# Kernel tuning notes

Measured on AMD Instinct MI355X. Metric: run time of the kernel, lower is better.

Reference implementation:

```python
import jax, jax.numpy as jnp
import numpy as np

NUM_HEADS = 16
HEAD_DIM = 64  # att_output_dim // num_heads = 1024 // 16


def setup_inputs() -> dict:
    key = jax.random.key(0)
    ks = jax.random.split(key, 7)
    B, S, D_IN, D_OUT = 4, 2048, 1024, 1024
    std = 1.0 / np.sqrt(D_IN)
    return {
        "ts10_input": jax.random.normal(ks[0], (B, S, D_IN), dtype=jnp.float32),
        "Wq": jax.random.uniform(ks[1], (D_IN, D_OUT), jnp.float32, -std, std),
        "bq": jax.random.uniform(ks[2], (D_OUT,), jnp.float32, -std, std),
        "Wk": jax.random.uniform(ks[3], (D_IN, D_OUT), jnp.float32, -std, std),
        "bk": jax.random.uniform(ks[4], (D_OUT,), jnp.float32, -std, std),
        "Wv": jax.random.uniform(ks[5], (D_IN, D_OUT), jnp.float32, -std, std),
        "bv": jax.random.uniform(ks[6], (D_OUT,), jnp.float32, -std, std),
        "mask": 1,
    }


def reference(ts10_input, Wq, bq, Wk, bk, Wv, bv, mask):
    B, S, _ = ts10_input.shape
    H, Dh = NUM_HEADS, HEAD_DIM

    def split_heads(x):  # (B,S,H*Dh) -> (B,H,S,Dh)
        return x.reshape(B, S, H, Dh).transpose(0, 2, 1, 3)

    q = split_heads(ts10_input @ Wq + bq)
    k = split_heads(ts10_input @ Wk + bk)
    v = split_heads(ts10_input @ Wv + bv)

    scores = jnp.einsum("bhqd,bhkd->bhqk", q, k) / jnp.sqrt(jnp.float32(Dh))
    if mask:
        causal = jnp.tril(jnp.ones((S, S), dtype=bool))  # keep lower triangle incl diag
        scores = jnp.where(causal, scores, -jnp.inf)
    probs = jax.nn.softmax(scores, axis=-1)
    ctx = jnp.einsum("bhqk,bhkd->bhqd", probs, v)
    return ctx.transpose(0, 2, 1, 3).reshape(B, S, H * Dh)
```

## Files before the change

### kernel.cpp

```cpp
#include <hip/hip_runtime.h>

typedef __bf16 bf16x8 __attribute__((ext_vector_type(8)));
typedef __bf16 bf16x4 __attribute__((ext_vector_type(4)));
typedef short s16x4 __attribute__((ext_vector_type(4)));
typedef float f32x4 __attribute__((ext_vector_type(4)));
typedef unsigned short u16x8 __attribute__((ext_vector_type(8)));
typedef unsigned short u16x4 __attribute__((ext_vector_type(4)));
typedef unsigned int u32x2 __attribute__((ext_vector_type(2)));
typedef unsigned int __attribute__((address_space(1))) as1_uint;
typedef unsigned int __attribute__((address_space(3))) as3_uint;

#define S_LEN 2048
#define NB 4
#define NH 16
#define HD 64
#define DM 1024

#define Q_SCALE 0.18033688011112042f

__device__ __forceinline__ unsigned short f2bf(float f) {
  union { float f; unsigned int u; } v; v.f = f;
  unsigned int r = v.u + 0x7fffu + ((v.u >> 16) & 1u);
  return (unsigned short)(r >> 16);
}

__device__ __forceinline__ unsigned int fbits(float f) {
  union { float f; unsigned int u; } v; v.f = f;
  return v.u;
}

__device__ __forceinline__ f32x4 mfma16(u16x4 a, u16x4 b, f32x4 c) {
#if __has_builtin(__builtin_amdgcn_mfma_f32_16x16x16_bf16)
  return __builtin_amdgcn_mfma_f32_16x16x16_bf16(
      __builtin_bit_cast(bf16x4, a), __builtin_bit_cast(bf16x4, b), c, 0, 0, 0);
#else
  return __builtin_amdgcn_mfma_f32_16x16x16bf16_1k(
      __builtin_bit_cast(s16x4, a), __builtin_bit_cast(s16x4, b), c, 0, 0, 0);
#endif
}

__global__ __launch_bounds__(256) void cvt_x(const float* __restrict__ x,
                                             unsigned short* __restrict__ xb) {
  int i = (blockIdx.x * 256 + threadIdx.x) * 8;
  f32x4 a = *(const f32x4*)(x + i);
  f32x4 b = *(const f32x4*)(x + i + 4);
  u16x8 o;
  o[0] = f2bf(a[0]); o[1] = f2bf(a[1]); o[2] = f2bf(a[2]); o[3] = f2bf(a[3]);
  o[4] = f2bf(b[0]); o[5] = f2bf(b[1]); o[6] = f2bf(b[2]); o[7] = f2bf(b[3]);
  *(u16x8*)(xb + i) = o;
}

__global__ __launch_bounds__(256) void cvt_wt(const float* __restrict__ Wq,
                                              const float* __restrict__ Wk,
                                              const float* __restrict__ Wv,
                                              unsigned short* __restrict__ wt) {
  const float* W = (blockIdx.z == 0) ? Wq : (blockIdx.z == 1) ? Wk : Wv;
  unsigned short* WT = wt + (size_t)blockIdx.z * DM * DM;
  __shared__ float tile[32][33];
  int tx = threadIdx.x & 31, ty = threadIdx.x >> 5;
  int k0 = blockIdx.x * 32, n0 = blockIdx.y * 32;
#pragma unroll
  for (int i = 0; i < 4; ++i)
    tile[ty + 8 * i][tx] = W[(size_t)(k0 + ty + 8 * i) * DM + n0 + tx];
  __syncthreads();
#pragma unroll
  for (int i = 0; i < 4; ++i)
    WT[(size_t)(n0 + ty + 8 * i) * DM + k0 + tx] = f2bf(tile[tx][ty + 8 * i]);
}

__global__ __launch_bounds__(256) void qkv_gemm(const unsigned short* __restrict__ xb,
                                                const unsigned short* __restrict__ wt,
                                                const float* __restrict__ bq,
                                                const float* __restrict__ bk,
                                                const float* __restrict__ bv,
                                                unsigned short* __restrict__ qo,
                                                unsigned short* __restrict__ ko,
                                                unsigned short* __restrict__ vto) {
  const int z = blockIdx.z;
  const unsigned short* WT = wt + (size_t)z * DM * DM;
  const float* bias = (z == 0) ? bq : (z == 1) ? bk : bv;
  const int m0 = blockIdx.x * 128;
  const int n0 = blockIdx.y * 128;
  __shared__ __align__(16) unsigned short Al[128 * 32];
  __shared__ __align__(16) unsigned short Bl[128 * 32];
  const int tid = threadIdx.x;
  const int wave = tid >> 6, lane = tid & 63, quad = lane >> 4, lw = lane & 15;
  const int wm = (wave >> 1) * 64, wn = (wave & 1) * 64;

  f32x4 acc[4][4];
#pragma unroll
  for (int mt = 0; mt < 4; ++mt)
#pragma unroll
    for (int nt = 0; nt < 4; ++nt) acc[mt][nt] = (f32x4){0.f, 0.f, 0.f, 0.f};

  for (int k0 = 0; k0 < DM; k0 += 32) {
    __syncthreads();
#pragma unroll
    for (int i = 0; i < 2; ++i) {
      int c = i * 256 + tid;
      int row = c >> 2;
      int scn = (c & 3) ^ ((row >> 1) & 3);
      const unsigned short* ga = xb + (size_t)(m0 + row) * DM + k0 + scn * 8;
      __builtin_amdgcn_global_load_lds((const as1_uint*)ga, (as3_uint*)(Al + c * 8), 16, 0, 0);
      const unsigned short* gb = WT + (size_t)(n0 + row) * DM + k0 + scn * 8;
      __builtin_amdgcn_global_load_lds((const as1_uint*)gb, (as3_uint*)(Bl + c * 8), 16, 0, 0);
    }
    __syncthreads();
    bf16x8 af[4], bfr[4];
#pragma unroll
    for (int mt = 0; mt < 4; ++mt) {
      int r = wm + mt * 16 + lw;
      af[mt] = *(const bf16x8*)(Al + r * 32 + (quad ^ ((r >> 1) & 3)) * 8);
    }
#pragma unroll
    for (int nt = 0; nt < 4; ++nt) {
      int r = wn + nt * 16 + lw;
      bfr[nt] = *(const bf16x8*)(Bl + r * 32 + (quad ^ ((r >> 1) & 3)) * 8);
    }
#pragma unroll
    for (int mt = 0; mt < 4; ++mt)
#pragma unroll
      for (int nt = 0; nt < 4; ++nt)
        acc[mt][nt] = __builtin_amdgcn_mfma_f32_16x16x32_bf16(af[mt], bfr[nt], acc[mt][nt], 0, 0, 0);
  }

  float bias4[4];
#pragma unroll
  for (int nt = 0; nt < 4; ++nt) bias4[nt] = bias[n0 + wn + nt * 16 + lw];

  if (z < 2) {
    unsigned short* dst = (z == 0) ? qo : ko;
    const float sc = (z == 0) ? Q_SCALE : 1.0f;
#pragma unroll
    for (int mt = 0; mt < 4; ++mt) {
#pragma unroll
      for (int nt = 0; nt < 4; ++nt) {
        int n = n0 + wn + nt * 16 + lw;
        int h = n >> 6, d = n & 63;
#pragma unroll
        for (int r = 0; r < 4; ++r) {
          int m = m0 + wm + mt * 16 + quad * 4 + r;
          int b = m >> 11, s = m & 2047;
          dst[((size_t)(b * NH + h) * S_LEN + s) * HD + d] = f2bf((acc[mt][nt][r] + bias4[nt]) * sc);
        }
      }
    }
  } else {
#pragma unroll
    for (int mt = 0; mt < 4; ++mt) {
#pragma unroll
      for (int nt = 0; nt < 4; ++nt) {
        int n = n0 + wn + nt * 16 + lw;
        int h = n >> 6, d = n & 63;
        int mb = m0 + wm + mt * 16 + quad * 4;
        int b = mb >> 11, s = mb & 2047;
        u16x4 pk;
#pragma unroll
        for (int r = 0; r < 4; ++r) pk[r] = f2bf(acc[mt][nt][r] + bias4[nt]);
        *(u16x4*)(vto + ((size_t)(b * NH + h) * HD + d) * S_LEN + s) = pk;
      }
    }
  }
}

__global__ __launch_bounds__(256, 4) void attn(const unsigned short* __restrict__ Qb,
                                               const unsigned short* __restrict__ Kb,
                                               const unsigned short* __restrict__ Vtb,
                                               float* __restrict__ out) {
  const int flat = blockIdx.x;
  const int bh_lo = flat & 7;
  const int qpair = (flat >> 3) & 15;
  const int bh_hi = flat >> 7;
  const int bh = bh_lo + 8 * bh_hi;
  const int b = bh >> 4, h = bh & 15;
  const int tid = threadIdx.x;
  const int wave = tid >> 6, lane = tid & 63;
  const int quad = lane >> 4, lw = lane & 15;
  const int qlo = qpair * 64;
  const int qhi = (31 - qpair) * 64;
  const unsigned short* Qp = Qb + (size_t)bh * S_LEN * HD;
  const unsigned short* Kp = Kb + (size_t)bh * S_LEN * HD;
  const unsigned short* Vp = Vtb + (size_t)bh * HD * S_LEN;

  __shared__ __align__(16) unsigned short Kl[2][64 * 64];
  __shared__ __align__(16) unsigned short Vl[2][64 * 64];

  bf16x8 aq[2][2];
#pragma unroll
  for (int rg = 0; rg < 2; ++rg) {
    const int qbase = rg ? qhi : qlo;
#pragma unroll
    for (int kc = 0; kc < 2; ++kc)
      aq[rg][kc] = *(const bf16x8*)(Qp + (size_t)(qbase + wave * 16 + lw) * HD + kc * 32 + quad * 8);
  }

  u16x4 ones4;
#pragma unroll
  for (int i = 0; i < 4; ++i) ones4[i] = 0x3F80;

  f32x4 accO[2][4];
  f32x4 accL[2];
#pragma unroll
  for (int rg = 0; rg < 2; ++rg) {
    accL[rg] = (f32x4){0.f, 0.f, 0.f, 0.f};
#pragma unroll
    for (int dg = 0; dg < 4; ++dg) accO[rg][dg] = (f32x4){0.f, 0.f, 0.f, 0.f};
  }

  const int qr0 = qlo + wave * 16 + lw;
  const int qr1 = qhi + wave * 16 + lw;

  const int T = 32 - qpair;

  {
#pragma unroll
    for (int i = 0; i < 2; ++i) {
      int idx = i * 256 + tid;
      int r = idx >> 3, c = (idx & 7) ^ (r & 7);
      __builtin_amdgcn_global_load_lds((const as1_uint*)(Kp + (size_t)r * HD + c * 8),
                                       (as3_uint*)(Kl[0] + idx * 8), 16, 0, 0);
      __builtin_amdgcn_global_load_lds((const as1_uint*)(Vp + (size_t)r * S_LEN + c * 8),
                                       (as3_uint*)(Vl[0] + idx * 8), 16, 0, 0);
    }
  }

  for (int t = 0; t < T; ++t) {
    const int kv = t * 64;
    const int cur = t & 1;
    __syncthreads();

    if (t + 1 < T) {
      const int kvn = kv + 64;
#pragma unroll
      for (int i = 0; i < 2; ++i) {
        int idx = i * 256 + tid;
        int r = idx >> 3, c = (idx & 7) ^ (r & 7);
        __builtin_amdgcn_global_load_lds((const as1_uint*)(Kp + (size_t)(kvn + r) * HD + c * 8),
                                         (as3_uint*)(Kl[cur ^ 1] + idx * 8), 16, 0, 0);
        __builtin_amdgcn_global_load_lds((const as1_uint*)(Vp + (size_t)r * S_LEN + kvn + c * 8),
                                         (as3_uint*)(Vl[cur ^ 1] + idx * 8), 16, 0, 0);
      }
    }

    const bool a0 = (t <= qpair);
    const bool d0 = (t == qpair);
    const bool d1 = (t == T - 1);

#pragma unroll
    for (int g = 0; g < 4; ++g) {
      const unsigned short* kp = Kl[cur] + (g * 16 + lw) * 64;
      const int sw = lw & 7;
      bf16x8 kf0 = *(const bf16x8*)(kp + ((quad ^ sw) * 8));
      bf16x8 kf1 = *(const bf16x8*)(kp + (((4 + quad) ^ sw) * 8));

      u16x4 pf[2];
#pragma unroll
      for (int rg = 0; rg < 2; ++rg) {
        if (rg == 0 && !a0) continue;
        f32x4 s = (f32x4){0.f, 0.f, 0.f, 0.f};
        s = __builtin_amdgcn_mfma_f32_16x16x32_bf16(kf0, aq[rg][0], s, 0, 0, 0);
        s = __builtin_amdgcn_mfma_f32_16x16x32_bf16(kf1, aq[rg][1], s, 0, 0, 0);
        const bool dg_ = rg ? d1 : d0;
        const int qr = rg ? qr1 : qr0;
        if (dg_) {
#pragma unroll
          for (int r = 0; r < 4; ++r) {
            float e = __builtin_amdgcn_exp2f(s[r]);
            s[r] = (kv + g * 16 + quad * 4 + r > qr) ? 0.f : e;
          }
        } else {
#pragma unroll
          for (int r = 0; r < 4; ++r) s[r] = __builtin_amdgcn_exp2f(s[r]);
        }
        u32x2 pk;
        pk[0] = (fbits(s[1]) & 0xFFFF0000u) | (fbits(s[0]) >> 16);
        pk[1] = (fbits(s[3]) & 0xFFFF0000u) | (fbits(s[2]) >> 16);
        pf[rg] = __builtin_bit_cast(u16x4, pk);
      }

#pragma unroll
      for (int dg = 0; dg < 4; ++dg) {
        const int row = dg * 16 + lw;
        const int slot = (2 * g + (quad >> 1)) ^ (lw & 7);
        u16x4 vf = *(const u16x4*)(Vl[cur] + row * 64 + slot * 8 + (quad & 1) * 4);
        if (a0) accO[0][dg] = mfma16(pf[0], vf, accO[0][dg]);
        accO[1][dg] = mfma16(pf[1], vf, accO[1][dg]);
      }
      if (a0) accL[0] = mfma16(pf[0], ones4, accL[0]);
      accL[1] = mfma16(pf[1], ones4, accL[1]);
    }
  }

#pragma unroll
  for (int rg = 0; rg < 2; ++rg) {
    const int qbase = rg ? qhi : qlo;
    float* op = out + ((size_t)b * S_LEN + qbase + wave * 16 + quad * 4) * DM + h * HD + lw;
#pragma unroll
    for (int r = 0; r < 4; ++r) {
      float inv = 1.0f / accL[rg][r];
#pragma unroll
      for (int dg = 0; dg < 4; ++dg) op[(size_t)r * DM + dg * 16] = accO[rg][dg][r] * inv;
    }
  }
}

extern "C" void kernel_launch(void* const* d_in, const int* in_sizes, int n_in,
                              void* d_out, int out_size, void* d_ws, size_t ws_size,
                              hipStream_t stream) {
  const float* x = (const float*)d_in[0];
  const float* Wq = (const float*)d_in[1];
  const float* bq = (const float*)d_in[2];
  const float* Wk = (const float*)d_in[3];
  const float* bk = (const float*)d_in[4];
  const float* Wv = (const float*)d_in[5];
  const float* bv = (const float*)d_in[6];
  float* out = (float*)d_out;

  char* ws = (char*)d_ws;
  unsigned short* xb = (unsigned short*)(ws + 0);
  unsigned short* wt = (unsigned short*)(ws + 16777216);
  unsigned short* qb = (unsigned short*)(ws + 23068672);
  unsigned short* kb = (unsigned short*)(ws + 39845888);
  unsigned short* vt = (unsigned short*)(ws + 56623104);

  hipLaunchKernelGGL(cvt_x, dim3(4096), dim3(256), 0, stream, x, xb);
  hipLaunchKernelGGL(cvt_wt, dim3(32, 32, 3), dim3(256), 0, stream, Wq, Wk, Wv, wt);
  hipLaunchKernelGGL(qkv_gemm, dim3(64, 8, 3), dim3(256), 0, stream,
                     xb, wt, bq, bk, bv, qb, kb, vt);
  hipLaunchKernelGGL(attn, dim3(1024), dim3(256), 0, stream, qb, kb, vt, out);
}
```

Baseline: 224.8 us.

## Double K-step in QKV GEMM and stage epilogue through LDS for vector stores

The QKV projection GEMM now loads 64-wide K slices per iteration with an 8-way XOR swizzle, which halves the number of barrier pairs per tile. The epilogue writes bias-added bf16 results into a padded LDS tile, then each thread emits 16-byte coalesced global stores for Q/K and the transposed V, replacing scattered 2-byte and 8-byte stores. Launch bounds request 4 blocks per CU. LDS use grows to about 34 KB per block, which may limit occupancy, and the epilogue gains an extra barrier.

```diff
diff --git a/kernel.cpp b/kernel.cpp
--- a/kernel.cpp
+++ b/kernel.cpp
@@ -7,6 +7,7 @@
 typedef unsigned short u16x8 __attribute__((ext_vector_type(8)));
 typedef unsigned short u16x4 __attribute__((ext_vector_type(4)));
 typedef unsigned int u32x2 __attribute__((ext_vector_type(2)));
+typedef unsigned int u32x4 __attribute__((ext_vector_type(4)));
 typedef unsigned int __attribute__((address_space(1))) as1_uint;
 typedef unsigned int __attribute__((address_space(3))) as3_uint;
 
@@ -68,21 +69,22 @@
     WT[(size_t)(n0 + ty + 8 * i) * DM + k0 + tx] = f2bf(tile[tx][ty + 8 * i]);
 }
 
-__global__ __launch_bounds__(256) void qkv_gemm(const unsigned short* __restrict__ xb,
-                                                const unsigned short* __restrict__ wt,
-                                                const float* __restrict__ bq,
-                                                const float* __restrict__ bk,
-                                                const float* __restrict__ bv,
-                                                unsigned short* __restrict__ qo,
-                                                unsigned short* __restrict__ ko,
-                                                unsigned short* __restrict__ vto) {
+__global__ __launch_bounds__(256, 4) void qkv_gemm(const unsigned short* __restrict__ xb,
+                                                   const unsigned short* __restrict__ wt,
+                                                   const float* __restrict__ bq,
+                                                   const float* __restrict__ bk,
+                                                   const float* __restrict__ bv,
+                                                   unsigned short* __restrict__ qo,
+                                                   unsigned short* __restrict__ ko,
+                                                   unsigned short* __restrict__ vto) {
   const int z = blockIdx.z;
   const unsigned short* WT = wt + (size_t)z * DM * DM;
   const float* bias = (z == 0) ? bq : (z == 1) ? bk : bv;
   const int m0 = blockIdx.x * 128;
   const int n0 = blockIdx.y * 128;
-  __shared__ __align__(16) unsigned short Al[128 * 32];
-  __shared__ __align__(16) unsigned short Bl[128 * 32];
+  __shared__ __align__(16) unsigned short Lds[128 * 136];
+  unsigned short* Al = Lds;
+  unsigned short* Bl = Lds + 128 * 64;
   const int tid = threadIdx.x;
   const int wave = tid >> 6, lane = tid & 63, quad = lane >> 4, lw = lane & 15;
   const int wm = (wave >> 1) * 64, wn = (wave & 1) * 64;
@@ -93,72 +95,99 @@
 #pragma unroll
     for (int nt = 0; nt < 4; ++nt) acc[mt][nt] = (f32x4){0.f, 0.f, 0.f, 0.f};
 
-  for (int k0 = 0; k0 < DM; k0 += 32) {
-    __syncthreads();
-#pragma unroll
-    for (int i = 0; i < 2; ++i) {
-      int c = i * 256 + tid;
-      int row = c >> 2;
-      int scn = (c & 3) ^ ((row >> 1) & 3);
-      const unsigned short* ga = xb + (size_t)(m0 + row) * DM + k0 + scn * 8;
-      __builtin_amdgcn_global_load_lds((const as1_uint*)ga, (as3_uint*)(Al + c * 8), 16, 0, 0);
-      const unsigned short* gb = WT + (size_t)(n0 + row) * DM + k0 + scn * 8;
-      __builtin_amdgcn_global_load_lds((const as1_uint*)gb, (as3_uint*)(Bl + c * 8), 16, 0, 0);
-    }
-    __syncthreads();
-    bf16x8 af[4], bfr[4];
-#pragma unroll
-    for (int mt = 0; mt < 4; ++mt) {
-      int r = wm + mt * 16 + lw;
-      af[mt] = *(const bf16x8*)(Al + r * 32 + (quad ^ ((r >> 1) & 3)) * 8);
-    }
-#pragma unroll
-    for (int nt = 0; nt < 4; ++nt) {
-      int r = wn + nt * 16 + lw;
-      bfr[nt] = *(const bf16x8*)(Bl + r * 32 + (quad ^ ((r >> 1) & 3)) * 8);
-    }
+  for (int k0 = 0; k0 < DM; k0 += 64) {
+    __syncthreads();
+#pragma unroll
+    for (int i = 0; i < 4; ++i) {
+      int idx = i * 256 + tid;
+      int r = idx >> 3, cp = idx & 7;
+      int cl = cp ^ (r & 7);
+      const unsigned short* ga = xb + (size_t)(m0 + r) * DM + k0 + cl * 8;
+      __builtin_amdgcn_global_load_lds((const as1_uint*)ga, (as3_uint*)(Al + idx * 8), 16, 0, 0);
+      const unsigned short* gb = WT + (size_t)(n0 + r) * DM + k0 + cl * 8;
+      __builtin_amdgcn_global_load_lds((const as1_uint*)gb, (as3_uint*)(Bl + idx * 8), 16, 0, 0);
+    }
+    __syncthreads();
+#pragma unroll
+    for (int kc = 0; kc < 2; ++kc) {
+      bf16x8 af[4], bfr[4];
+#pragma unroll
+      for (int mt = 0; mt < 4; ++mt) {
+        int r = wm + mt * 16 + lw;
+        int cp = (kc * 4 + quad) ^ (r & 7);
+        af[mt] = *(const bf16x8*)(Al + r * 64 + cp * 8);
+      }
+#pragma unroll
+      for (int nt = 0; nt < 4; ++nt) {
+        int r = wn + nt * 16 + lw;
+        int cp = (kc * 4 + quad) ^ (r & 7);
+        bfr[nt] = *(const bf16x8*)(Bl + r * 64 + cp * 8);
+      }
+#pragma unroll
+      for (int mt = 0; mt < 4; ++mt)
+#pragma unroll
+        for (int nt = 0; nt < 4; ++nt)
+          acc[mt][nt] = __builtin_amdgcn_mfma_f32_16x16x32_bf16(af[mt], bfr[nt], acc[mt][nt], 0, 0, 0);
+    }
+  }
+
+  float bias4[4];
+#pragma unroll
+  for (int nt = 0; nt < 4; ++nt) bias4[nt] = bias[n0 + wn + nt * 16 + lw];
+
+  __syncthreads();
+
+  if (z < 2) {
+    const float sc = (z == 0) ? Q_SCALE : 1.0f;
 #pragma unroll
     for (int mt = 0; mt < 4; ++mt)
 #pragma unroll
-      for (int nt = 0; nt < 4; ++nt)
-        acc[mt][nt] = __builtin_amdgcn_mfma_f32_16x16x32_bf16(af[mt], bfr[nt], acc[mt][nt], 0, 0, 0);
-  }
-
-  float bias4[4];
-#pragma unroll
-  for (int nt = 0; nt < 4; ++nt) bias4[nt] = bias[n0 + wn + nt * 16 + lw];
-
-  if (z < 2) {
+      for (int nt = 0; nt < 4; ++nt) {
+        int n = wn + nt * 16 + lw;
+#pragma unroll
+        for (int r = 0; r < 4; ++r) {
+          int m = wm + mt * 16 + quad * 4 + r;
+          Lds[m * 136 + n] = f2bf((acc[mt][nt][r] + bias4[nt]) * sc);
+        }
+      }
+    __syncthreads();
     unsigned short* dst = (z == 0) ? qo : ko;
-    const float sc = (z == 0) ? Q_SCALE : 1.0f;
-#pragma unroll
-    for (int mt = 0; mt < 4; ++mt) {
+    const int rr = tid >> 1;
+    const int cbase = (tid & 1) * 64;
+    const int m = m0 + rr;
+    const int b = m >> 11, s = m & 2047;
+#pragma unroll
+    for (int ch = 0; ch < 8; ++ch) {
+      int cc = cbase + ch * 8;
+      int n = n0 + cc;
+      int h = n >> 6, d = n & 63;
+      u32x4 v = *(const u32x4*)(Lds + rr * 136 + cc);
+      *(u32x4*)(dst + ((size_t)(b * NH + h) * S_LEN + s) * HD + d) = v;
+    }
+  } else {
+#pragma unroll
+    for (int mt = 0; mt < 4; ++mt)
 #pragma unroll
       for (int nt = 0; nt < 4; ++nt) {
-        int n = n0 + wn + nt * 16 + lw;
-        int h = n >> 6, d = n & 63;
-#pragma unroll
-        for (int r = 0; r < 4; ++r) {
-          int m = m0 + wm + mt * 16 + quad * 4 + r;
-          int b = m >> 11, s = m & 2047;
-          dst[((size_t)(b * NH + h) * S_LEN + s) * HD + d] = f2bf((acc[mt][nt][r] + bias4[nt]) * sc);
-        }
-      }
-    }
-  } else {
-#pragma unroll
-    for (int mt = 0; mt < 4; ++mt) {
-#pragma unroll
-      for (int nt = 0; nt < 4; ++nt) {
-        int n = n0 + wn + nt * 16 + lw;
-        int h = n >> 6, d = n & 63;
-        int mb = m0 + wm + mt * 16 + quad * 4;
-        int b = mb >> 11, s = mb & 2047;
+        int n = wn + nt * 16 + lw;
+        int mb = wm + mt * 16 + quad * 4;
         u16x4 pk;
 #pragma unroll
         for (int r = 0; r < 4; ++r) pk[r] = f2bf(acc[mt][nt][r] + bias4[nt]);
-        *(u16x4*)(vto + ((size_t)(b * NH + h) * HD + d) * S_LEN + s) = pk;
-      }
+        *(u16x4*)(Lds + n * 136 + mb) = pk;
+      }
+    __syncthreads();
+    const int rr = tid >> 1;
+    const int cbase = (tid & 1) * 64;
+    const int n = n0 + rr;
+    const int h = n >> 6, d = n & 63;
+#pragma unroll
+    for (int ch = 0; ch < 8; ++ch) {
+      int cc = cbase + ch * 8;
+      int m = m0 + cc;
+      int b = m >> 11, s = m & 2047;
+      u32x4 v = *(const u32x4*)(Lds + rr * 136 + cc);
+      *(u32x4*)(vto + ((size_t)(b * NH + h) * HD + d) * S_LEN + s) = v;
     }
   }
 }
```

New measurement: 230.1 us. 2.4% more time.
